# Optimization experiments

Measured on AMD Instinct MI355X. Metric: run time of the kernel, lower is better.

Reference implementation:

```python
import jax, jax.numpy as jnp
import numpy as np

N = 1024
E = 10
IN = 78
NOTE = 128
BEAT = 64
MEAS = 32
S = NOTE + (BEAT + MEAS) * 2  # 320, GatedGraph state width
SEC = NOTE                    # secondary_size
HEADS = 8
NPB = 4    # notes per beat
BPM = 4    # beats per measure
NB = N // NPB                 # 256 beats
NM = N // (NPB * BPM)         # 64 measures
SEQ_ITER = 2
GRAPH_ITER = 2


def setup_inputs() -> dict:
    key = jax.random.key(0)
    ks = iter(jax.random.split(key, 64))
    def rn(shape, s=0.05):
        return jax.random.normal(next(ks), shape, jnp.float32) * s
    nodes = jax.random.normal(next(ks), (1, N, IN), jnp.float32)
    adjacency = (jax.random.uniform(next(ks), (E, N, N)) < 0.01).astype(jnp.float32)
    beat_numbers = jnp.arange(N, dtype=jnp.int32) // NPB
    measure_numbers = jnp.arange(N, dtype=jnp.int32) // (NPB * BPM)
    inp = dict(nodes=nodes, adjacency=adjacency,
               beat_numbers=beat_numbers, measure_numbers=measure_numbers,
               num_beats=NB, num_measures=NM)
    inp['note_fc_w'] = rn((IN, NOTE)); inp['note_fc_b'] = rn((NOTE,))
    for g in ('g1', 'g2'):
        inp[g+'_wz'] = rn((E, S, SEC)); inp[g+'_wr'] = rn((E, S, SEC)); inp[g+'_wh'] = rn((E, S, SEC))
        inp[g+'_uz'] = rn((SEC, SEC)); inp[g+'_ur'] = rn((SEC, SEC)); inp[g+'_uh'] = rn((SEC, SEC))
        inp[g+'_bz'] = rn((SEC,)); inp[g+'_br'] = rn((SEC,)); inp[g+'_bh'] = rn((SEC,))
    inp['gb_w'] = rn((S, S)); inp['gb_b'] = rn((S,))
    inp['batt_w'] = rn((2*NOTE, 2*NOTE)); inp['batt_b'] = rn((2*NOTE,)); inp['batt_c'] = rn((HEADS, 2*NOTE//HEADS), 1.0)
    inp['matt_w'] = rn((2*BEAT, 2*BEAT)); inp['matt_b'] = rn((2*BEAT,)); inp['matt_c'] = rn((HEADS, 2*BEAT//HEADS), 1.0)
    inp['blstm_wi_f'] = rn((4*BEAT, 2*NOTE)); inp['blstm_wh_f'] = rn((4*BEAT, BEAT)); inp['blstm_b_f'] = rn((4*BEAT,))
    inp['blstm_wi_b'] = rn((4*BEAT, 2*NOTE)); inp['blstm_wh_b'] = rn((4*BEAT, BEAT)); inp['blstm_b_b'] = rn((4*BEAT,))
    inp['mlstm_wi_f'] = rn((4*MEAS, 2*BEAT)); inp['mlstm_wh_f'] = rn((4*MEAS, MEAS)); inp['mlstm_b_f'] = rn((4*MEAS,))
    inp['mlstm_wi_b'] = rn((4*MEAS, 2*BEAT)); inp['mlstm_wh_b'] = rn((4*MEAS, MEAS)); inp['mlstm_b_b'] = rn((4*MEAS,))
    return inp


def gated_graph(x, adj, wz, wr, wh, uz, ur, uh, bz, br, bh, n_iter, sec):
    # x: (N, S); adj: (E, N, N). Faithful to virtuosoNet GatedGraph (batch=1).
    for _ in range(n_iter):
        act = jnp.einsum('emn,mf->enf', adj, x)            # adj[e]^T @ x
        mz = jnp.einsum('enf,efs->ns', act, wz)            # sum over edge types
        mr = jnp.einsum('enf,efs->ns', act, wr)
        mh = jnp.einsum('enf,efs->ns', act, wh)
        xs = x[:, -sec:]
        z = jax.nn.sigmoid(mz + xs @ uz + bz)
        r = jax.nn.sigmoid(mr + xs @ ur + br)
        h = jnp.tanh(mh + (r * xs) @ uh + bh)
        new_sec = (1.0 - z) * xs + r * h                   # virtuosoNet update rule
        x = jnp.concatenate([x[:, :-sec], new_sec], axis=1)
    return x


def seg_attention(x, seg, G, W, b, c):
    # ContextAttention pooled per ragged segment. x: (M, D), c: (H, hd)
    M, D = x.shape
    H, hd = c.shape
    a = jnp.tanh(x @ W + b).reshape(M, H, hd)
    sim = jnp.einsum('mhd,hd->mh', a, c)
    mx = jax.ops.segment_max(sim, seg, num_segments=G)
    w = jnp.exp(sim - mx[seg])
    den = jax.ops.segment_sum(w, seg, num_segments=G)
    w = w / den[seg]
    out = jax.ops.segment_sum(x.reshape(M, H, hd) * w[:, :, None], seg, num_segments=G)
    return out.reshape(G, D)


def lstm_dir(x, wi, wh, b, H):
    def step(carry, xt):
        h, c = carry
        g = wi @ xt + wh @ h + b
        i, f, gg, o = jnp.split(g, 4)
        c = jax.nn.sigmoid(f) * c + jax.nn.sigmoid(i) * jnp.tanh(gg)
        h = jax.nn.sigmoid(o) * jnp.tanh(c)
        return (h, c), h
    init = (jnp.zeros((H,), x.dtype), jnp.zeros((H,), x.dtype))
    _, hs = jax.lax.scan(step, init, x)
    return hs


def bilstm(x, wif, whf, bf, wib, whb, bb, H):
    fw = lstm_dir(x, wif, whf, bf, H)
    bw = lstm_dir(x[::-1], wib, whb, bb, H)[::-1]
    return jnp.concatenate([fw, bw], axis=-1)


def reference(nodes, adjacency, note_fc_w, note_fc_b,
              g1_wz, g1_wr, g1_wh, g1_uz, g1_ur, g1_uh, g1_bz, g1_br, g1_bh,
              gb_w, gb_b,
              g2_wz, g2_wr, g2_wh, g2_uz, g2_ur, g2_uh, g2_bz, g2_br, g2_bh,
              batt_w, batt_b, batt_c, matt_w, matt_b, matt_c,
              blstm_wi_f, blstm_wh_f, blstm_b_f, blstm_wi_b, blstm_wh_b, blstm_b_b,
              mlstm_wi_f, mlstm_wh_f, mlstm_b_f, mlstm_wi_b, mlstm_wh_b, mlstm_b_b,
              beat_numbers, measure_numbers, num_beats, num_measures):
    n = nodes.shape[1]
    x0 = jnp.tanh(nodes[0] @ note_fc_w + note_fc_b)                     # (N, NOTE)
    notes_hidden = jnp.concatenate(
        [jnp.zeros((n, (BEAT + MEAS) * 2), jnp.float32), x0], axis=1)  # (N, S)
    # measure index of each beat = measure at the first note of that beat
    beat_to_meas = jax.ops.segment_min(measure_numbers, beat_numbers, num_segments=num_beats)
    nh2 = notes_hidden
    for _ in range(SEQ_ITER):
        nh = gated_graph(notes_hidden, adjacency, g1_wz, g1_wr, g1_wh,
                         g1_uz, g1_ur, g1_uh, g1_bz, g1_br, g1_bh, GRAPH_ITER, SEC)
        nb = jax.nn.relu(nh @ gb_w + gb_b)
        nh2 = gated_graph(nb, adjacency, g2_wz, g2_wr, g2_wh,
                          g2_uz, g2_ur, g2_uh, g2_bz, g2_br, g2_bh, GRAPH_ITER, SEC)
        cat = jnp.concatenate([nh[:, -SEC:], nh2[:, -SEC:]], axis=-1)   # (N, 2*NOTE)
        beat_nodes = seg_attention(cat, beat_numbers, num_beats, batt_w, batt_b, batt_c)
        beat_hidden = bilstm(beat_nodes, blstm_wi_f, blstm_wh_f, blstm_b_f,
                             blstm_wi_b, blstm_wh_b, blstm_b_b, BEAT)   # (NB, 2*BEAT)
        measure_nodes = seg_attention(beat_hidden, beat_to_meas, num_measures, matt_w, matt_b, matt_c)
        measure_hidden = bilstm(measure_nodes, mlstm_wi_f, mlstm_wh_f, mlstm_b_f,
                                mlstm_wi_b, mlstm_wh_b, mlstm_b_b, MEAS)  # (NM, 2*MEAS)
        beat_spanned = beat_hidden[beat_numbers]                        # (N, 2*BEAT)
        meas_spanned = measure_hidden[measure_numbers]                  # (N, 2*MEAS)
        notes_hidden = jnp.concatenate([beat_spanned, meas_spanned, nh[:, -SEC:]], axis=-1)
    final = jnp.concatenate([notes_hidden, nh2[:, -SEC:]], axis=-1)     # (N, S + NOTE)
    return final[None]  # 'total_note_cat': (1, N, 448)
```

## Files before the change

### kernel.cpp

```cpp
#include <hip/hip_runtime.h>
#include <math.h>


#define NN    1024
#define EE    10
#define INDIM 78
#define SS    320
#define SECD  128
#define NB    256
#define NM    64
#define CAP   64

typedef float v2f __attribute__((ext_vector_type(2)));

__device__ __forceinline__ void pkfma(v2f& a, v2f x, v2f y){
    asm("v_pk_fma_f32 %0, %1, %2, %0" : "+v"(a) : "v"(x), "v"(y));
}
__device__ __forceinline__ void pkfma_blo(v2f& a, v2f x, v2f b){
    asm("v_pk_fma_f32 %0, %1, %2, %0 op_sel:[0,0,0] op_sel_hi:[1,0,1]"
        : "+v"(a) : "v"(x), "v"(b));
}
__device__ __forceinline__ void pkfma_bhi(v2f& a, v2f x, v2f b){
    asm("v_pk_fma_f32 %0, %1, %2, %0 op_sel:[0,1,0] op_sel_hi:[1,1,1]"
        : "+v"(a) : "v"(x), "v"(b));
}

#define LO2(F) ((v2f){F.x, F.y})
#define HI2(F) ((v2f){F.z, F.w})

__device__ __forceinline__ float fsig(float x){
    return __builtin_amdgcn_rcpf(1.f + __expf(-x));
}
__device__ __forceinline__ float ftanh(float x){
    return 1.f - 2.f*__builtin_amdgcn_rcpf(1.f + __expf(2.f*x));
}

__global__ void k_note_fc(const float* __restrict__ nodes, const float* __restrict__ W,
                          const float* __restrict__ b, float* __restrict__ nh){
    int n = blockIdx.x, s = threadIdx.x;
    __shared__ float xrow[INDIM];
    if (s < INDIM) xrow[s] = nodes[n*INDIM + s];
    __syncthreads();
    float acc = b[s];
    for (int k = 0; k < INDIM; ++k) acc += xrow[k]*W[k*128 + s];
    nh[n*SS + 192 + s] = ftanh(acc);
    nh[n*SS + s] = 0.f;
    if (s < 64) nh[n*SS + 128 + s] = 0.f;
}

__global__ void k_csr_build(const float* __restrict__ adj, int* __restrict__ cnt,
                            int* __restrict__ idx){
    int em = blockIdx.x;
    int e = em / NN, m = em % NN;
    const float4* row4 = (const float4*)(adj + (size_t)em * NN);
    int q = threadIdx.x;
    float4 v = row4[q];
    int n0 = q*4;
    if (v.x != 0.f){ int p = atomicAdd(&cnt[e*NN + n0+0], 1); if (p < CAP) idx[((size_t)e*NN + n0+0)*CAP + p] = m; }
    if (v.y != 0.f){ int p = atomicAdd(&cnt[e*NN + n0+1], 1); if (p < CAP) idx[((size_t)e*NN + n0+1)*CAP + p] = m; }
    if (v.z != 0.f){ int p = atomicAdd(&cnt[e*NN + n0+2], 1); if (p < CAP) idx[((size_t)e*NN + n0+2)*CAP + p] = m; }
    if (v.w != 0.f){ int p = atomicAdd(&cnt[e*NN + n0+3], 1); if (p < CAP) idx[((size_t)e*NN + n0+3)*CAP + p] = m; }
}

__global__ void k_gather_act_rng(const float* __restrict__ x, const int* __restrict__ cnt,
                                 const int* __restrict__ idx, float* __restrict__ act,
                                 int F0){
    int en = blockIdx.x, f = F0 + threadIdx.x;
    int c = cnt[en]; if (c > CAP) c = CAP;
    const int* lst = idx + (size_t)en*CAP;
    float acc = 0.f;
    for (int j = 0; j < c; ++j) acc += x[lst[j]*SS + f];
    act[(size_t)en*SS + f] = acc;
}

template<int K0, int K1>
__global__ __launch_bounds__(256) void k_gate_gemm_rng(const float* __restrict__ act,
        const float* __restrict__ wz, const float* __restrict__ wr,
        const float* __restrict__ wh, float* __restrict__ part){
    __shared__ float A[32*36];
    __shared__ float B[32*132];
    int nt = blockIdx.x, g = blockIdx.y, z = blockIdx.z;
    const float* W = (g==0) ? wz : ((g==1) ? wr : wh);
    int tid = threadIdx.x;
    int tx = tid & 31;
    int ty = tid >> 5;
    v2f acc[2][4];
    #pragma unroll
    for (int i=0;i<2;i++)
        #pragma unroll
        for (int j=0;j<4;j++) acc[i][j] = (v2f){0.f,0.f};
    for (int eh = 0; eh < 2; ++eh){
        int e = z*2 + eh;
        const float* Ae = act + (size_t)e*NN*SS + (size_t)nt*32*SS;
        const float* We = W   + (size_t)e*SS*SECD;
        for (int kc = K0; kc < K1; kc += 32){
            {
                int r  = tid >> 3;
                int k4 = (tid & 7) << 2;
                float4 v = *(const float4*)(Ae + r*SS + kc + k4);
                A[(k4+0)*36 + r] = v.x; A[(k4+1)*36 + r] = v.y;
                A[(k4+2)*36 + r] = v.z; A[(k4+3)*36 + r] = v.w;
            }
            #pragma unroll
            for (int i=0;i<4;i++){
                int lin4 = tid + i*256;
                int kk = lin4 >> 5;
                int c4 = (lin4 & 31) << 2;
                *((float4*)(B + kk*132 + c4)) = *(const float4*)(We + (kc+kk)*SECD + c4);
            }
            __syncthreads();
            #pragma unroll 8
            for (int k=0;k<32;k++){
                const v2f* A2 = (const v2f*)(A + k*36 + ty*4);
                v2f a01 = A2[0], a23 = A2[1];
                float4 b = *(const float4*)(B + k*132 + tx*4);
                v2f b01 = {b.x, b.y}, b23 = {b.z, b.w};
                pkfma_blo(acc[0][0], a01, b01); pkfma_bhi(acc[0][1], a01, b01);
                pkfma_blo(acc[0][2], a01, b23); pkfma_bhi(acc[0][3], a01, b23);
                pkfma_blo(acc[1][0], a23, b01); pkfma_bhi(acc[1][1], a23, b01);
                pkfma_blo(acc[1][2], a23, b23); pkfma_bhi(acc[1][3], a23, b23);
            }
            __syncthreads();
        }
    }
    float* P = part + ((size_t)z*NN + (size_t)nt*32)*384 + g*SECD;
    int r0 = ty*4;
    *(float4*)(P + (size_t)(r0+0)*384 + tx*4) =
        make_float4(acc[0][0].x, acc[0][1].x, acc[0][2].x, acc[0][3].x);
    *(float4*)(P + (size_t)(r0+1)*384 + tx*4) =
        make_float4(acc[0][0].y, acc[0][1].y, acc[0][2].y, acc[0][3].y);
    *(float4*)(P + (size_t)(r0+2)*384 + tx*4) =
        make_float4(acc[1][0].x, acc[1][1].x, acc[1][2].x, acc[1][3].x);
    *(float4*)(P + (size_t)(r0+3)*384 + tx*4) =
        make_float4(acc[1][0].y, acc[1][1].y, acc[1][2].y, acc[1][3].y);
}

__global__ void k_gru(float* __restrict__ x, const float* __restrict__ part, int nsp,
        const float* __restrict__ uz, const float* __restrict__ ur, const float* __restrict__ uh,
        const float* __restrict__ bz, const float* __restrict__ br, const float* __restrict__ bh){
    int n0 = blockIdx.x*2, s = threadIdx.x;
    __shared__ float xs[2][SECD], rx[2][SECD];
    #pragma unroll
    for (int j=0;j<2;j++) xs[j][s] = x[(n0+j)*SS + 192 + s];
    __syncthreads();
    float mz[2]={0,0}, mr[2]={0,0}, mh[2]={0,0};
    for (int sp=0; sp<nsp; sp++){
        const float* Pp = part + ((size_t)sp*NN + n0)*384;
        #pragma unroll
        for (int j=0;j<2;j++){
            mz[j] += Pp[j*384 + s];
            mr[j] += Pp[j*384 + 128 + s];
            mh[j] += Pp[j*384 + 256 + s];
        }
    }
    float dz[2]={0,0}, dr[2]={0,0};
    for (int k=0;k<SECD;k++){
        float wz_ = uz[k*SECD + s], wr_ = ur[k*SECD + s];
        #pragma unroll
        for (int j=0;j<2;j++){ float xv = xs[j][k]; dz[j] += xv*wz_; dr[j] += xv*wr_; }
    }
    float zz[2], rr[2];
    #pragma unroll
    for (int j=0;j<2;j++){
        zz[j] = fsig(mz[j] + dz[j] + bz[s]);
        rr[j] = fsig(mr[j] + dr[j] + br[s]);
        rx[j][s] = rr[j]*xs[j][s];
    }
    __syncthreads();
    float dh[2]={0,0};
    for (int k=0;k<SECD;k++){
        float wh_ = uh[k*SECD + s];
        #pragma unroll
        for (int j=0;j<2;j++) dh[j] += rx[j][k]*wh_;
    }
    #pragma unroll
    for (int j=0;j<2;j++){
        float h = ftanh(mh[j] + dh[j] + bh[s]);
        x[(n0+j)*SS + 192 + s] = (1.f - zz[j])*xs[j][s] + rr[j]*h;
    }
}

__global__ void k_gb(const float* __restrict__ nh, const float* __restrict__ W,
                     const float* __restrict__ b, float* __restrict__ nb){
    int n0 = blockIdx.x*4, s = threadIdx.x;
    __shared__ float xr_t[SS*4];
    {
        float v0 = nh[(n0+0)*SS + s], v1 = nh[(n0+1)*SS + s];
        float v2 = nh[(n0+2)*SS + s], v3 = nh[(n0+3)*SS + s];
        *(float4*)(xr_t + s*4) = make_float4(v0,v1,v2,v3);
    }
    __syncthreads();
    float bv = b[s];
    v2f a01={bv,bv}, a23={bv,bv};
    for (int k=0;k<SS;k++){
        float wv = W[k*SS + s];
        v2f ws = {wv, wv};
        const v2f* xp = (const v2f*)(xr_t + k*4);
        pkfma(a01, xp[0], ws);
        pkfma(a23, xp[1], ws);
    }
    nb[(n0+0)*SS + s] = fmaxf(a01.x, 0.f);
    nb[(n0+1)*SS + s] = fmaxf(a01.y, 0.f);
    nb[(n0+2)*SS + s] = fmaxf(a23.x, 0.f);
    nb[(n0+3)*SS + s] = fmaxf(a23.y, 0.f);
}

__global__ __launch_bounds__(256) void k_batt_fused(
        const float* __restrict__ nh, const float* __restrict__ nh2,
        const float* __restrict__ W, const float* __restrict__ b,
        const float* __restrict__ cvec,
        const float* __restrict__ wi_f, const float* __restrict__ b_f,
        const float* __restrict__ wi_b, const float* __restrict__ b_b,
        float* __restrict__ gf, float* __restrict__ gbo){
    int g = blockIdx.x, s = threadIdx.x;
    __shared__ float xr_t[256*4];
    __shared__ float simw[4][8];
    __shared__ float wgt[4][8];
    __shared__ float bnode[256];
    {
        float c0,c1,c2,c3;
        if (s < 128){
            c0 = nh[(g*4+0)*SS + 192 + s]; c1 = nh[(g*4+1)*SS + 192 + s];
            c2 = nh[(g*4+2)*SS + 192 + s]; c3 = nh[(g*4+3)*SS + 192 + s];
        } else {
            c0 = nh2[(g*4+0)*SS + 64 + s]; c1 = nh2[(g*4+1)*SS + 64 + s];
            c2 = nh2[(g*4+2)*SS + 64 + s]; c3 = nh2[(g*4+3)*SS + 64 + s];
        }
        *(float4*)(xr_t + s*4) = make_float4(c0,c1,c2,c3);
    }
    __syncthreads();
    float bias = b[s];
    v2f ac01 = {bias,bias}, ac23 = {bias,bias};
    for (int k=0;k<256;k++){
        float wv = W[k*256 + s];
        v2f ws = {wv, wv};
        const v2f* xp = (const v2f*)(xr_t + k*4);
        pkfma(ac01, xp[0], ws);
        pkfma(ac23, xp[1], ws);
    }
    float accj[4] = {ac01.x, ac01.y, ac23.x, ac23.y};
    float cv = cvec[s];
    int h = s >> 5;
    #pragma unroll
    for (int j=0;j<4;j++){
        float p = ftanh(accj[j])*cv;
        #pragma unroll
        for (int off=16; off>0; off>>=1) p += __shfl_down(p, off);
        if ((s & 31) == 0) simw[j][h] = p;
    }
    __syncthreads();
    if (s < 8){
        float v0=simw[0][s], v1=simw[1][s], v2=simw[2][s], v3=simw[3][s];
        float mx = fmaxf(fmaxf(v0,v1), fmaxf(v2,v3));
        float e0=__expf(v0-mx), e1=__expf(v1-mx), e2=__expf(v2-mx), e3=__expf(v3-mx);
        float den = e0+e1+e2+e3;
        wgt[0][s]=e0/den; wgt[1][s]=e1/den; wgt[2][s]=e2/den; wgt[3][s]=e3/den;
    }
    __syncthreads();
    float4 xs4 = *(const float4*)(xr_t + s*4);
    float o = xs4.x*wgt[0][h] + xs4.y*wgt[1][h] + xs4.z*wgt[2][h] + xs4.w*wgt[3][h];
    bnode[s] = o;
    __syncthreads();
    v2f afA = {b_f[s], 0.f}, afB = {0.f, 0.f};
    v2f abA = {b_b[s], 0.f}, abB = {0.f, 0.f};
    const v2f* wfp = (const v2f*)(wi_f + (size_t)s*256);
    const v2f* wbp = (const v2f*)(wi_b + (size_t)s*256);
    const v2f* bp  = (const v2f*)bnode;
    for (int k2=0;k2<128;k2+=2){
        v2f x01 = bp[k2], x23 = bp[k2+1];
        pkfma(afA, wfp[k2], x01); pkfma(afB, wfp[k2+1], x23);
        pkfma(abA, wbp[k2], x01); pkfma(abB, wbp[k2+1], x23);
    }
    gf [g*256 + s] = (afA.x + afA.y) + (afB.x + afB.y);
    gbo[g*256 + s] = (abA.x + abA.y) + (abB.x + abB.y);
}

__global__ __launch_bounds__(128) void k_matt_fused(
        const float* __restrict__ bh,
        const float* __restrict__ W, const float* __restrict__ b,
        const float* __restrict__ cvec,
        const float* __restrict__ wi_f, const float* __restrict__ b_f,
        const float* __restrict__ wi_b, const float* __restrict__ b_b,
        float* __restrict__ gf, float* __restrict__ gbo){
    int g = blockIdx.x, s = threadIdx.x;
    __shared__ float xr_t[128*4];
    __shared__ float simw[4][8];
    __shared__ float wgt[4][8];
    __shared__ float mnode[128];
    {
        float c0 = bh[(g*4+0)*128 + s], c1 = bh[(g*4+1)*128 + s];
        float c2 = bh[(g*4+2)*128 + s], c3 = bh[(g*4+3)*128 + s];
        *(float4*)(xr_t + s*4) = make_float4(c0,c1,c2,c3);
    }
    __syncthreads();
    float bias = b[s];
    v2f ac01 = {bias,bias}, ac23 = {bias,bias};
    for (int k=0;k<128;k++){
        float wv = W[k*128 + s];
        v2f ws = {wv, wv};
        const v2f* xp = (const v2f*)(xr_t + k*4);
        pkfma(ac01, xp[0], ws);
        pkfma(ac23, xp[1], ws);
    }
    float accj[4] = {ac01.x, ac01.y, ac23.x, ac23.y};
    float cv = cvec[s];
    int h = s >> 4;
    #pragma unroll
    for (int j=0;j<4;j++){
        float p = ftanh(accj[j])*cv;
        #pragma unroll
        for (int off=8; off>0; off>>=1) p += __shfl_down(p, off);
        if ((s & 15) == 0) simw[j][h] = p;
    }
    __syncthreads();
    if (s < 8){
        float v0=simw[0][s], v1=simw[1][s], v2=simw[2][s], v3=simw[3][s];
        float mx = fmaxf(fmaxf(v0,v1), fmaxf(v2,v3));
        float e0=__expf(v0-mx), e1=__expf(v1-mx), e2=__expf(v2-mx), e3=__expf(v3-mx);
        float den = e0+e1+e2+e3;
        wgt[0][s]=e0/den; wgt[1][s]=e1/den; wgt[2][s]=e2/den; wgt[3][s]=e3/den;
    }
    __syncthreads();
    float4 xs4 = *(const float4*)(xr_t + s*4);
    float o = xs4.x*wgt[0][h] + xs4.y*wgt[1][h] + xs4.z*wgt[2][h] + xs4.w*wgt[3][h];
    mnode[s] = o;
    __syncthreads();
    v2f afA = {b_f[s], 0.f}, afB = {0.f, 0.f};
    v2f abA = {b_b[s], 0.f}, abB = {0.f, 0.f};
    const v2f* wfp = (const v2f*)(wi_f + (size_t)s*128);
    const v2f* wbp = (const v2f*)(wi_b + (size_t)s*128);
    const v2f* bp  = (const v2f*)mnode;
    for (int k2=0;k2<64;k2+=2){
        v2f x01 = bp[k2], x23 = bp[k2+1];
        pkfma(afA, wfp[k2], x01); pkfma(afB, wfp[k2+1], x23);
        pkfma(abA, wbp[k2], x01); pkfma(abB, wbp[k2+1], x23);
    }
    gf [g*128 + s] = (afA.x + afA.y) + (afB.x + afB.y);
    gbo[g*128 + s] = (abA.x + abA.y) + (abB.x + abB.y);
}

__global__ __launch_bounds__(256)
__attribute__((amdgpu_waves_per_eu(1, 1)))
void k_lstm_rec64(
        const float* __restrict__ gin_f, const float* __restrict__ wh_f,
        const float* __restrict__ gin_b, const float* __restrict__ wh_b,
        float* __restrict__ hid ){
    const int H = 64, T = 256;
    int dir = blockIdx.x;
    const float* gin = dir ? gin_b : gin_f;
    const float* wh  = dir ? wh_b  : wh_f;
    int gi = threadIdx.x;
    int l  = gi & 63;
    const v2f* wp = (const v2f*)(wh + (size_t)gi*H);
    v2f w00=wp[0], w01=wp[1], w02=wp[2], w03=wp[3], w04=wp[4], w05=wp[5], w06=wp[6], w07=wp[7],
        w08=wp[8], w09=wp[9], w10=wp[10],w11=wp[11],w12=wp[12],w13=wp[13],w14=wp[14],w15=wp[15],
        w16=wp[16],w17=wp[17],w18=wp[18],w19=wp[19],w20=wp[20],w21=wp[21],w22=wp[22],w23=wp[23],
        w24=wp[24],w25=wp[25],w26=wp[26],w27=wp[27],w28=wp[28],w29=wp[29],w30=wp[30],w31=wp[31];
    __shared__ __align__(16) float hs[H];
    __shared__ float gsum[2][4*H];
    float c = 0.f;
    if (gi < H) hs[gi] = 0.f;
    __syncthreads();
    float gcur = gin[(dir ? (T-1) : 0)*4*H + gi];
    for (int step=0; step<T; step++){
        int t = dir ? (T-1-step) : step;
        float gnext = 0.f;
        if (step+1 < T) gnext = gin[(dir ? (T-2-step) : (step+1))*4*H + gi];
        const float4* hv = (const float4*)hs;
        float4 H0=hv[0],  H1=hv[1],  H2=hv[2],  H3=hv[3];
        float4 H4=hv[4],  H5=hv[5],  H6=hv[6],  H7=hv[7];
        float4 H8=hv[8],  H9=hv[9],  H10=hv[10],H11=hv[11];
        float4 H12=hv[12],H13=hv[13],H14=hv[14],H15=hv[15];
        v2f A0={gcur,0.f}, A1={0.f,0.f}, A2={0.f,0.f}, A3={0.f,0.f};
        pkfma(A0,w00,LO2(H0));  pkfma(A1,w01,HI2(H0));  pkfma(A2,w02,LO2(H1));  pkfma(A3,w03,HI2(H1));
        pkfma(A0,w04,LO2(H2));  pkfma(A1,w05,HI2(H2));  pkfma(A2,w06,LO2(H3));  pkfma(A3,w07,HI2(H3));
        pkfma(A0,w08,LO2(H4));  pkfma(A1,w09,HI2(H4));  pkfma(A2,w10,LO2(H5));  pkfma(A3,w11,HI2(H5));
        pkfma(A0,w12,LO2(H6));  pkfma(A1,w13,HI2(H6));  pkfma(A2,w14,LO2(H7));  pkfma(A3,w15,HI2(H7));
        pkfma(A0,w16,LO2(H8));  pkfma(A1,w17,HI2(H8));  pkfma(A2,w18,LO2(H9));  pkfma(A3,w19,HI2(H9));
        pkfma(A0,w20,LO2(H10)); pkfma(A1,w21,HI2(H10)); pkfma(A2,w22,LO2(H11)); pkfma(A3,w23,HI2(H11));
        pkfma(A0,w24,LO2(H12)); pkfma(A1,w25,HI2(H12)); pkfma(A2,w26,LO2(H13)); pkfma(A3,w27,HI2(H13));
        pkfma(A0,w28,LO2(H14)); pkfma(A1,w29,HI2(H14)); pkfma(A2,w30,LO2(H15)); pkfma(A3,w31,HI2(H15));
        float* gs = gsum[step & 1];
        gs[gi] = ((A0.x+A0.y) + (A1.x+A1.y)) + ((A2.x+A2.y) + (A3.x+A3.y));
        __syncthreads();
        float ig = gs[l], fg = gs[H+l], gg = gs[2*H+l], og = gs[3*H+l];
        c = fsig(fg)*c + fsig(ig)*ftanh(gg);
        float hn = fsig(og)*ftanh(c);
        hs[l] = hn;
        if (gi < H) hid[t*2*H + dir*H + gi] = hn;
        gcur = gnext;
    }
}

__global__ __launch_bounds__(64)
__attribute__((amdgpu_waves_per_eu(1, 1)))
void k_lstm_rec32(
        const float* __restrict__ gin_f, const float* __restrict__ wh_f,
        const float* __restrict__ gin_b, const float* __restrict__ wh_b,
        float* __restrict__ hid ){
    const int H = 32, T = 64;
    int dir = blockIdx.x;
    const float* gin = dir ? gin_b : gin_f;
    const float* wh  = dir ? wh_b  : wh_f;
    int gi = threadIdx.x;
    v2f wA[16], wB[16];
    {
        const v2f* rA = (const v2f*)(wh + (size_t)(     gi)*H);
        const v2f* rB = (const v2f*)(wh + (size_t)(64 + gi)*H);
        #pragma unroll
        for (int k=0;k<16;k++){ wA[k]=rA[k]; wB[k]=rB[k]; }
    }
    __shared__ __align__(16) float hs[H];
    float c = 0.f;
    if (gi < H) hs[gi] = 0.f;
    __syncthreads();
    const float* gp = gin + gi;
    int ts0 = dir ? (T-1) : 0, ts1 = dir ? (T-2) : 1;
    float g0 = gp[ts0*128], g1 = gp[ts0*128 + 64];
    float n0 = gp[ts1*128], n1 = gp[ts1*128 + 64];
    bool lo = (gi < H);
    for (int step=0; step<T; step++){
        int t = dir ? (T-1-step) : step;
        float p0=0.f, p1=0.f;
        if (step+2 < T){
            int tp = dir ? (T-3-step) : (step+2);
            p0 = gp[tp*128]; p1 = gp[tp*128 + 64];
        }
        v2f aA = {g0, 0.f}, aB = {g1, 0.f};
        const float4* hv = (const float4*)hs;
        #pragma unroll
        for (int k=0;k<8;k++){
            float4 h4 = hv[k];
            pkfma(aA, wA[2*k],   LO2(h4));
            pkfma(aB, wB[2*k],   LO2(h4));
            pkfma(aA, wA[2*k+1], HI2(h4));
            pkfma(aB, wB[2*k+1], HI2(h4));
        }
        float sA = aA.x + aA.y;
        float sB = aB.x + aB.y;
        float pA = __shfl(sA, gi ^ 32);
        float pB = __shfl(sB, gi ^ 32);
        float i_ = lo ? sA : pA;
        float f_ = lo ? pA : sA;
        float g_ = lo ? sB : pB;
        float o_ = lo ? pB : sB;
        c = fsig(f_)*c + fsig(i_)*ftanh(g_);
        float hn = fsig(o_)*ftanh(c);
        if (lo){
            hid[t*2*H + dir*H + gi] = hn;
            hs[gi] = hn;
        }
        g0 = n0; g1 = n1; n0 = p0; n1 = p1;
    }
}

__global__ void k_spans(float* __restrict__ nh, const float* __restrict__ bh,
                        const float* __restrict__ mh,
                        const int* __restrict__ bn, const int* __restrict__ mn){
    int n = blockIdx.x, s = threadIdx.x;
    float v;
    if (s < 128)      v = bh[bn[n]*128 + s];
    else if (s < 192) v = mh[mn[n]*64 + (s-128)];
    else              v = nh[n*SS + s];
    nh[n*SS + s] = v;
}

__global__ void k_spans_out(const float* __restrict__ bh, const float* __restrict__ mh,
                            const float* __restrict__ nh, const float* __restrict__ nh2,
                            const int* __restrict__ bn, const int* __restrict__ mn,
                            float* __restrict__ out){
    int n = blockIdx.x, s = threadIdx.x;
    float v;
    if (s < 128)      v = bh[bn[n]*128 + s];
    else if (s < 192) v = mh[mn[n]*64 + (s-128)];
    else if (s < 320) v = nh[n*SS + s];
    else              v = nh2[n*SS + 192 + (s-320)];
    out[n*448 + s] = v;
}

extern "C" void kernel_launch(void* const* d_in, const int* in_sizes, int n_in,
                              void* d_out, int out_size, void* d_ws, size_t ws_size,
                              hipStream_t stream) {
    const float* nodes    = (const float*)d_in[0];
    const float* adj      = (const float*)d_in[1];
    const int*   bn       = (const int*)  d_in[2];
    const int*   mn       = (const int*)  d_in[3];
    const float* fc_w     = (const float*)d_in[6];
    const float* fc_b     = (const float*)d_in[7];
    const float* g_wz[2]  = {(const float*)d_in[8],  (const float*)d_in[17]};
    const float* g_wr[2]  = {(const float*)d_in[9],  (const float*)d_in[18]};
    const float* g_wh[2]  = {(const float*)d_in[10], (const float*)d_in[19]};
    const float* g_uz[2]  = {(const float*)d_in[11], (const float*)d_in[20]};
    const float* g_ur[2]  = {(const float*)d_in[12], (const float*)d_in[21]};
    const float* g_uh[2]  = {(const float*)d_in[13], (const float*)d_in[22]};
    const float* g_bz[2]  = {(const float*)d_in[14], (const float*)d_in[23]};
    const float* g_br[2]  = {(const float*)d_in[15], (const float*)d_in[24]};
    const float* g_bh[2]  = {(const float*)d_in[16], (const float*)d_in[25]};
    const float* gb_w     = (const float*)d_in[26];
    const float* gb_b     = (const float*)d_in[27];
    const float* batt_w   = (const float*)d_in[28];
    const float* batt_b   = (const float*)d_in[29];
    const float* batt_c   = (const float*)d_in[30];
    const float* matt_w   = (const float*)d_in[31];
    const float* matt_b   = (const float*)d_in[32];
    const float* matt_c   = (const float*)d_in[33];
    const float* bwi_f    = (const float*)d_in[34];
    const float* bwh_f    = (const float*)d_in[35];
    const float* bb_f     = (const float*)d_in[36];
    const float* bwi_b    = (const float*)d_in[37];
    const float* bwh_b    = (const float*)d_in[38];
    const float* bb_b     = (const float*)d_in[39];
    const float* mwi_f    = (const float*)d_in[40];
    const float* mwh_f    = (const float*)d_in[41];
    const float* mb_f     = (const float*)d_in[42];
    const float* mwi_b    = (const float*)d_in[43];
    const float* mwh_b    = (const float*)d_in[44];
    const float* mb_b     = (const float*)d_in[45];
    float* out = (float*)d_out;

    float* W_   = (float*)d_ws;
    float* nh   = W_;
    float* nh2  = nh   + 327680;
    float* act  = nh2  + 327680;
    float* part = act  + 3276800;
    float* bgf  = part + 3932160;
    float* bgb  = bgf  + 65536;
    float* beat_hidden = bgb + 65536;
    float* mgf  = beat_hidden + 32768;
    float* mgb  = mgf  + 8192;
    float* meas_hidden = mgb + 8192;
    int*   cnt  = (int*)(meas_hidden + 4096);
    int*   idx  = cnt + 10240;

    float* part_s = part + 5*NN*384;

    hipMemsetAsync(cnt, 0, EE*NN*sizeof(int), stream);
    k_csr_build<<<EE*NN, 256, 0, stream>>>(adj, cnt, idx);
    k_note_fc<<<NN, 128, 0, stream>>>(nodes, fc_w, fc_b, nh);

    for (int si = 0; si < 2; ++si){
        for (int half = 0; half < 2; ++half){
            float* x = half ? nh2 : nh;
            int w = half;
            bool zerostatic = (si == 0 && half == 0);
            if (half == 1)
                k_gb<<<NN/4, SS, 0, stream>>>(nh, gb_w, gb_b, nh2);
            if (!zerostatic){
                k_gather_act_rng<<<EE*NN, 192, 0, stream>>>(x, cnt, idx, act, 0);
                k_gate_gemm_rng<0,192><<<dim3(32,3,5), 256, 0, stream>>>(
                        act, g_wz[w], g_wr[w], g_wh[w], part_s);
            }
            int nsp = zerostatic ? 5 : 10;
            for (int it = 0; it < 2; ++it){
                k_gather_act_rng<<<EE*NN, 128, 0, stream>>>(x, cnt, idx, act, 192);
                k_gate_gemm_rng<192,320><<<dim3(32,3,5), 256, 0, stream>>>(
                        act, g_wz[w], g_wr[w], g_wh[w], part);
                k_gru<<<NN/2, 128, 0, stream>>>(x, part, nsp,
                        g_uz[w], g_ur[w], g_uh[w], g_bz[w], g_br[w], g_bh[w]);
            }
        }
        k_batt_fused<<<NB, 256, 0, stream>>>(nh, nh2, batt_w, batt_b, batt_c,
                                             bwi_f, bb_f, bwi_b, bb_b, bgf, bgb);
        k_lstm_rec64<<<2, 256, 0, stream>>>(bgf, bwh_f, bgb, bwh_b, beat_hidden);
        k_matt_fused<<<NM, 128, 0, stream>>>(beat_hidden, matt_w, matt_b, matt_c,
                                             mwi_f, mb_f, mwi_b, mb_b, mgf, mgb);
        k_lstm_rec32<<<2, 64, 0, stream>>>(mgf, mwh_f, mgb, mwh_b, meas_hidden);
        if (si == 0)
            k_spans<<<NN, SS, 0, stream>>>(nh, beat_hidden, meas_hidden, bn, mn);
        else
            k_spans_out<<<NN, 448, 0, stream>>>(beat_hidden, meas_hidden, nh, nh2,
                                                bn, mn, out);
    }
}
```

Baseline: 1.085 ms.

## Vectorize neighbor gathers, merge static/dynamic gather, shuffle-based LSTM gate exchange

```diff
diff --git a/kernel.cpp b/kernel.cpp
--- a/kernel.cpp
+++ b/kernel.cpp
@@ -62,15 +62,34 @@
     if (v.w != 0.f){ int p = atomicAdd(&cnt[e*NN + n0+3], 1); if (p < CAP) idx[((size_t)e*NN + n0+3)*CAP + p] = m; }
 }
 
-__global__ void k_gather_act_rng(const float* __restrict__ x, const int* __restrict__ cnt,
-                                 const int* __restrict__ idx, float* __restrict__ act,
-                                 int F0){
-    int en = blockIdx.x, f = F0 + threadIdx.x;
+__global__ void k_gather_full(const float* __restrict__ x, const int* __restrict__ cnt,
+                              const int* __restrict__ idx, float* __restrict__ act){
+    int en = blockIdx.x*4 + threadIdx.x/80;
+    int q  = threadIdx.x % 80;
     int c = cnt[en]; if (c > CAP) c = CAP;
     const int* lst = idx + (size_t)en*CAP;
-    float acc = 0.f;
-    for (int j = 0; j < c; ++j) acc += x[lst[j]*SS + f];
-    act[(size_t)en*SS + f] = acc;
+    float4 acc = {0.f,0.f,0.f,0.f};
+    const float* xb = x + q*4;
+    for (int j = 0; j < c; ++j){
+        float4 v = *(const float4*)(xb + (size_t)lst[j]*SS);
+        acc.x += v.x; acc.y += v.y; acc.z += v.z; acc.w += v.w;
+    }
+    *(float4*)(act + (size_t)en*SS + q*4) = acc;
+}
+
+__global__ void k_gather_dyn(const float* __restrict__ x, const int* __restrict__ cnt,
+                             const int* __restrict__ idx, float* __restrict__ act){
+    int en = blockIdx.x*8 + (threadIdx.x >> 5);
+    int q  = threadIdx.x & 31;
+    int c = cnt[en]; if (c > CAP) c = CAP;
+    const int* lst = idx + (size_t)en*CAP;
+    float4 acc = {0.f,0.f,0.f,0.f};
+    const float* xb = x + 192 + q*4;
+    for (int j = 0; j < c; ++j){
+        float4 v = *(const float4*)(xb + (size_t)lst[j]*SS);
+        acc.x += v.x; acc.y += v.y; acc.z += v.z; acc.w += v.w;
+    }
+    *(float4*)(act + (size_t)en*SS + 192 + q*4) = acc;
 }
 
 template<int K0, int K1>
@@ -350,23 +369,28 @@
     const float* gin = dir ? gin_b : gin_f;
     const float* wh  = dir ? wh_b  : wh_f;
     int gi = threadIdx.x;
-    int l  = gi & 63;
-    const v2f* wp = (const v2f*)(wh + (size_t)gi*H);
+    int w  = gi >> 6;
+    int j  = gi & 63;
+    int o  = j & 15;
+    int g  = j >> 4;
+    int l  = (w << 4) + o;
+    int row = (g << 6) + l;
+    const v2f* wp = (const v2f*)(wh + (size_t)row*H);
     v2f w00=wp[0], w01=wp[1], w02=wp[2], w03=wp[3], w04=wp[4], w05=wp[5], w06=wp[6], w07=wp[7],
         w08=wp[8], w09=wp[9], w10=wp[10],w11=wp[11],w12=wp[12],w13=wp[13],w14=wp[14],w15=wp[15],
         w16=wp[16],w17=wp[17],w18=wp[18],w19=wp[19],w20=wp[20],w21=wp[21],w22=wp[22],w23=wp[23],
         w24=wp[24],w25=wp[25],w26=wp[26],w27=wp[27],w28=wp[28],w29=wp[29],w30=wp[30],w31=wp[31];
-    __shared__ __align__(16) float hs[H];
-    __shared__ float gsum[2][4*H];
+    __shared__ __align__(16) float hsb[2][H];
     float c = 0.f;
-    if (gi < H) hs[gi] = 0.f;
-    __syncthreads();
-    float gcur = gin[(dir ? (T-1) : 0)*4*H + gi];
+    if (gi < H) hsb[0][gi] = 0.f;
+    __syncthreads();
+    const float* gp = gin + row;
+    float gcur = gp[(dir ? (T-1) : 0)*256];
     for (int step=0; step<T; step++){
         int t = dir ? (T-1-step) : step;
         float gnext = 0.f;
-        if (step+1 < T) gnext = gin[(dir ? (T-2-step) : (step+1))*4*H + gi];
-        const float4* hv = (const float4*)hs;
+        if (step+1 < T) gnext = gp[(dir ? (T-2-step) : (step+1))*256];
+        const float4* hv = (const float4*)hsb[step & 1];
         float4 H0=hv[0],  H1=hv[1],  H2=hv[2],  H3=hv[3];
         float4 H4=hv[4],  H5=hv[5],  H6=hv[6],  H7=hv[7];
         float4 H8=hv[8],  H9=hv[9],  H10=hv[10],H11=hv[11];
@@ -380,14 +404,18 @@
         pkfma(A0,w20,LO2(H10)); pkfma(A1,w21,HI2(H10)); pkfma(A2,w22,LO2(H11)); pkfma(A3,w23,HI2(H11));
         pkfma(A0,w24,LO2(H12)); pkfma(A1,w25,HI2(H12)); pkfma(A2,w26,LO2(H13)); pkfma(A3,w27,HI2(H13));
         pkfma(A0,w28,LO2(H14)); pkfma(A1,w29,HI2(H14)); pkfma(A2,w30,LO2(H15)); pkfma(A3,w31,HI2(H15));
-        float* gs = gsum[step & 1];
-        gs[gi] = ((A0.x+A0.y) + (A1.x+A1.y)) + ((A2.x+A2.y) + (A3.x+A3.y));
+        float val = ((A0.x+A0.y) + (A1.x+A1.y)) + ((A2.x+A2.y) + (A3.x+A3.y));
+        float i_ = __shfl(val, o);
+        float f_ = __shfl(val, o + 16);
+        float g_ = __shfl(val, o + 32);
+        float o_ = __shfl(val, o + 48);
+        c = fsig(f_)*c + fsig(i_)*ftanh(g_);
+        float hn = fsig(o_)*ftanh(c);
+        if (g == 0){
+            hsb[(step+1)&1][l] = hn;
+            hid[t*2*H + dir*H + l] = hn;
+        }
         __syncthreads();
-        float ig = gs[l], fg = gs[H+l], gg = gs[2*H+l], og = gs[3*H+l];
-        c = fsig(fg)*c + fsig(ig)*ftanh(gg);
-        float hn = fsig(og)*ftanh(c);
-        hs[l] = hn;
-        if (gi < H) hid[t*2*H + dir*H + gi] = hn;
         gcur = gnext;
     }
 }
@@ -545,14 +573,15 @@
             bool zerostatic = (si == 0 && half == 0);
             if (half == 1)
                 k_gb<<<NN/4, SS, 0, stream>>>(nh, gb_w, gb_b, nh2);
-            if (!zerostatic){
-                k_gather_act_rng<<<EE*NN, 192, 0, stream>>>(x, cnt, idx, act, 0);
-                k_gate_gemm_rng<0,192><<<dim3(32,3,5), 256, 0, stream>>>(
-                        act, g_wz[w], g_wr[w], g_wh[w], part_s);
-            }
             int nsp = zerostatic ? 5 : 10;
             for (int it = 0; it < 2; ++it){
-                k_gather_act_rng<<<EE*NN, 128, 0, stream>>>(x, cnt, idx, act, 192);
+                if (!zerostatic && it == 0){
+                    k_gather_full<<<EE*NN/4, 320, 0, stream>>>(x, cnt, idx, act);
+                    k_gate_gemm_rng<0,192><<<dim3(32,3,5), 256, 0, stream>>>(
+                            act, g_wz[w], g_wr[w], g_wh[w], part_s);
+                } else {
+                    k_gather_dyn<<<EE*NN/8, 256, 0, stream>>>(x, cnt, idx, act);
+                }
                 k_gate_gemm_rng<192,320><<<dim3(32,3,5), 256, 0, stream>>>(
                         act, g_wz[w], g_wr[w], g_wh[w], part);
                 k_gru<<<NN/2, 128, 0, stream>>>(x, part, nsp,
```

Measured after the change: 1.041 ms. 1.04x faster.
